# Kernel tuning notes

Hardware: AMD Instinct MI355X
Metric: run time of the kernel (lower is better)

## Reference

```python
import jax, jax.numpy as jnp
import numpy as np

TOPK = 10
HID = 512
RHID = 150
CH = 32


def _gru(x, Wi, Wh, bi, bh):
    """torch nn.GRU (1 layer, batch_first) with gate order r,z,n. x: [B,T,D]."""
    H = Wh.shape[1]
    xi = x @ Wi.T + bi  # [B,T,3H] precompute input projections

    def step(h, xt):
        gh = h @ Wh.T + bh
        r = jax.nn.sigmoid(xt[:, :H] + gh[:, :H])
        z = jax.nn.sigmoid(xt[:, H:2 * H] + gh[:, H:2 * H])
        n = jnp.tanh(xt[:, 2 * H:] + r * gh[:, 2 * H:])
        h_new = (1.0 - z) * n + z * h
        return h_new, h_new

    h0 = jnp.zeros((x.shape[0], H), x.dtype)
    hT, ys = jax.lax.scan(step, h0, jnp.swapaxes(xi, 0, 1))
    return jnp.swapaxes(ys, 0, 1), hT


def reference(window, emb, w_init, w_root, arma_b, Wi1, Wh1, bi1, bh1,
              Wi2, Wh2, bi2, bh2, W_fc, b_fc):
    B, T, N = window.shape
    # --- SingleEmbedding (post-warmup): cosine similarity + per-row top-k ---
    Wn = emb / jnp.clip(jnp.linalg.norm(emb, axis=1, keepdims=True), 1e-8, None)
    A = Wn @ Wn.T
    A = A * (1.0 - jnp.eye(N, dtype=A.dtype))  # fill_diagonal_(0)
    A = jnp.maximum(A, 0.0)                    # clamp(0)
    vals, idx = jax.lax.top_k(A, TOPK)         # [N, TOPK]
    # zero-valued edges kept with weight 0: identical math (zero degree/message contribution)
    src = jnp.repeat(jnp.arange(N), TOPK)      # edge source = row i
    dst = idx.reshape(-1)                      # edge dest = col j
    attr = vals.reshape(-1)
    # --- batch edges over B (offset b*N), then over T (offset t*B*N), as in torch code ---
    boff = jnp.arange(B) * N
    bsrc = (src[None, :] + boff[:, None]).reshape(-1)   # [B*E]
    bdst = (dst[None, :] + boff[:, None]).reshape(-1)
    battr = jnp.tile(attr, B)
    toff = jnp.arange(T) * (B * N)
    fsrc = (bsrc[None, :] + toff[:, None]).reshape(-1)  # [T*B*E]
    fdst = (bdst[None, :] + toff[:, None]).reshape(-1)
    fattr = jnp.tile(battr, T)
    Ntot = B * N * T
    # node layout (b, n, t): flat row = (b*N + n)*T + t  (faithful to torch view order)
    x = jnp.transpose(window, (0, 2, 1)).reshape(Ntot, 1)
    # --- ARMAConv: 1 stack, 1 layer, GELU, gcn_norm without self-loops ---
    deg = jax.ops.segment_sum(fattr, fdst, num_segments=Ntot)
    dinv = jnp.where(deg > 0, jax.lax.rsqrt(jnp.where(deg > 0, deg, 1.0)), 0.0)
    enorm = dinv[fsrc] * fattr * dinv[fdst]
    h = x @ w_init                                            # [Ntot, CH]
    agg = jax.ops.segment_sum(h[fsrc] * enorm[:, None], fdst, num_segments=Ntot)
    out = jax.nn.gelu(agg + x @ w_root + arma_b, approximate=False)
    # --- add node embedding, GRU encode ---
    xt = out.reshape(B, N, T, CH).transpose(0, 2, 1, 3) + emb  # [B,T,N,CH]
    xt = xt.reshape(B, T, N * CH)
    _, h_end = _gru(xt, Wi1, Wh1, bi1, bh1)                   # [B, HID]
    # --- ReconstructionModel: repeat_interleave(T, dim=1).view(B,T,-1) then GRU+fc ---
    hrep = jnp.repeat(h_end, T, axis=1).reshape(B, T, HID)
    dec, _ = _gru(hrep, Wi2, Wh2, bi2, bh2)                   # [B,T,RHID]
    return dec @ W_fc.T + b_fc


def setup_inputs():
    key = jax.random.key(0)
    ks = jax.random.split(key, 10)
    B, T, N = 32, 100, 150
    d_in = N * CH
    return {
        "window": jax.random.normal(ks[0], (B, T, N), jnp.float32),
        "emb": jax.random.normal(ks[1], (N, CH), jnp.float32) * 0.3,
        "w_init": jax.random.normal(ks[2], (1, CH), jnp.float32) * 0.5,
        "w_root": jax.random.normal(ks[3], (1, CH), jnp.float32) * 0.5,
        "arma_b": jnp.zeros((CH,), jnp.float32),
        "Wi1": jax.random.normal(ks[4], (3 * HID, d_in), jnp.float32) * (1.0 / np.sqrt(d_in)),
        "Wh1": jax.random.normal(ks[5], (3 * HID, HID), jnp.float32) * (1.0 / np.sqrt(HID)),
        "bi1": jnp.zeros((3 * HID,), jnp.float32),
        "bh1": jnp.zeros((3 * HID,), jnp.float32),
        "Wi2": jax.random.normal(ks[6], (3 * RHID, HID), jnp.float32) * (1.0 / np.sqrt(HID)),
        "Wh2": jax.random.normal(ks[7], (3 * RHID, RHID), jnp.float32) * (1.0 / np.sqrt(RHID)),
        "bi2": jnp.zeros((3 * RHID,), jnp.float32),
        "bh2": jnp.zeros((3 * RHID,), jnp.float32),
        "W_fc": jax.random.normal(ks[8], (N, RHID), jnp.float32) * (1.0 / np.sqrt(RHID)),
        "b_fc": jnp.zeros((N,), jnp.float32),
    }
```

## Files before the change

kernel.cpp:

```cpp
#include <hip/hip_runtime.h>
#include <hip/hip_fp16.h>
#include <math.h>

typedef _Float16 f16;
typedef _Float16 half8 __attribute__((ext_vector_type(8)));
typedef _Float16 half4 __attribute__((ext_vector_type(4)));
typedef float float4v __attribute__((ext_vector_type(4)));
typedef float float2v __attribute__((ext_vector_type(2)));
typedef unsigned int uint4v __attribute__((ext_vector_type(4)));

#define AS1 __attribute__((address_space(1)))
#define AS3 __attribute__((address_space(3)))

constexpr size_t alup(size_t x){ return (x + 255) & ~(size_t)255; }
constexpr size_t OFF_MT   = 0;
constexpr size_t OFF_DEG  = alup(OFF_MT + 150*150*4);
constexpr size_t OFF_HT0  = alup(OFF_DEG + 150*4);
constexpr size_t OFF_HT1  = alup(OFF_HT0 + (size_t)32*512*4);
constexpr size_t OFF_WI2P = alup(OFF_HT1 + (size_t)32*512*4);
constexpr size_t OFF_WFCP = alup(OFF_WI2P + (size_t)512*512*2);
constexpr size_t OFF_WH2P = alup(OFF_WFCP + (size_t)256*192*2);
constexpr size_t OFF_DECB = alup(OFF_WH2P + (size_t)512*160*2);
constexpr size_t ZONE_END = alup(OFF_DECB + (size_t)3200*192*2);
constexpr size_t OFF_EDST = ZONE_END;
constexpr size_t OFF_EVAL = alup(OFF_EDST + 1500*4);
constexpr size_t OFF_XF   = alup(OFF_EVAL + 1500*4);
constexpr size_t OFF_SS   = alup(OFF_XF + (size_t)480000*4);
constexpr size_t OFF_XT   = alup(OFF_SS + (size_t)480000*4);
constexpr size_t OFF_WI1H = alup(OFF_XT + (size_t)3200*4800*2);
constexpr size_t OFF_XI1  = alup(OFF_WI1H + (size_t)1536*4800*2);
constexpr size_t OFF_U    = alup(OFF_XI1 + (size_t)3200*1536*2);
constexpr size_t OFF_XI2  = alup(OFF_U + (size_t)3200*512*2);

static __device__ __forceinline__ float fsig(float x){ return 1.0f/(1.0f + __expf(-x)); }
static __device__ __forceinline__ float ftanh(float x){
    x = fminf(fmaxf(x, -15.f), 15.f);
    float e = __expf(2.0f*x);
    return (e - 1.0f)/(e + 1.0f);
}

__global__ void k_topk(const float* __restrict__ emb, int* __restrict__ EDST,
                       float* __restrict__ EVAL, float* __restrict__ DEG) {
    __shared__ float WnT[32*152];
    __shared__ float invn[160];
    __shared__ float As[160];
    int tid = threadIdx.x;
    int i = blockIdx.x;
    for (int idx = tid; idx < 4800; idx += 256) {
        int jj = idx >> 5, c = idx & 31;
        WnT[c*152 + jj] = emb[idx];
    }
    __syncthreads();
    if (tid < 150) {
        float s = 0.f;
        #pragma unroll
        for (int c = 0; c < 32; ++c) { float v = WnT[c*152 + tid]; s += v*v; }
        invn[tid] = 1.0f / fmaxf(sqrtf(s), 1e-8f);
    }
    __syncthreads();
    for (int idx = tid; idx < 4800; idx += 256) {
        int jj = idx >> 5, c = idx & 31;
        WnT[c*152 + jj] *= invn[jj];
    }
    __syncthreads();
    int j = tid;
    if (j < 150) {
        float a = 0.f;
        #pragma unroll
        for (int c = 0; c < 32; ++c) a += WnT[c*152 + i] * WnT[c*152 + j];
        a = (j == i) ? 0.f : fmaxf(a, 0.f);
        As[j] = a;
    }
    __syncthreads();
    if (j < 150) {
        float aj = As[j];
        int cnt = 0;
        for (int m = 0; m < 150; ++m) {
            float am = As[m];
            cnt += (am > aj) || (am == aj && m < j);
        }
        if (cnt < 10) {
            EDST[i*10 + cnt] = j;
            EVAL[i*10 + cnt] = aj;
            atomicAdd(&DEG[j], aj);
        }
    }
}

__global__ void k_prep(const int* __restrict__ EDST, const float* __restrict__ EVAL,
                       const float* __restrict__ DEG, float* __restrict__ MT,
                       const float* __restrict__ Wi1, f16* __restrict__ WI1H,
                       const float* __restrict__ Wi2, f16* __restrict__ WI2P,
                       const float* __restrict__ W_fc, f16* __restrict__ WFCP,
                       const float* __restrict__ Wh2, f16* __restrict__ WH2P,
                       const float* __restrict__ window, float* __restrict__ XF) {
    int b = blockIdx.x, tid = threadIdx.x;
    if (b == 0) {
        __shared__ float dinv[160];
        if (tid < 150) {
            float d = DEG[tid];
            dinv[tid] = (d > 0.f) ? rsqrtf(d) : 0.f;
        }
        __syncthreads();
        for (int e = tid; e < 1500; e += 256) {
            int src = e / 10;
            int dst = EDST[e];
            MT[src*150 + dst] = dinv[src] * EVAL[e] * dinv[dst];
        }
    } else if (b < 28801) {
        int idx = (b - 1)*256 + tid;
        WI1H[idx] = (f16)Wi1[idx];
    } else if (b < 29701) {
        int idx = (b - 28801)*256 + tid;
        WI2P[idx] = (f16)Wi2[idx];
    } else if (b < 29789) {
        int idx = (b - 29701)*256 + tid;
        if (idx < 22500) {
            int r = idx / 150, c = idx % 150;
            WFCP[r*192 + c] = (f16)W_fc[idx];
        }
    } else if (b < 30053) {
        int idx = (b - 29789)*256 + tid;
        if (idx < 67500) {
            int r = idx / 150, c = idx % 150;
            WH2P[r*160 + c] = (f16)Wh2[idx];
        }
    } else {
        int idx = (b - 30053)*256 + tid;
        float v = window[idx];
        int bb = idx / 15000;
        int r = idx % 15000;
        int t = r / 150, n = r % 150;
        XF[bb*15000 + n*100 + t] = v;
    }
}

__global__ void k_conv(const float* __restrict__ XF, const float* __restrict__ MT,
                       float* __restrict__ SS) {
    __shared__ float xs[152];
    int tid = threadIdx.x;
    int base = blockIdx.x * 150;
    if (tid < 150) xs[tid] = XF[base + tid];
    __syncthreads();
    if (tid < 150) {
        float s = 0.f;
        for (int m = 0; m < 150; ++m) s += MT[m*150 + tid] * xs[m];
        SS[base + tid] = s;
    }
}

__global__ void k_xt(const float* __restrict__ SS, const float* __restrict__ XF,
                     const float* __restrict__ w_init, const float* __restrict__ w_root,
                     const float* __restrict__ arma_b, const float* __restrict__ emb,
                     f16* __restrict__ xt) {
    __shared__ float ssl[152];
    __shared__ float xfl[152];
    int tid = threadIdx.x;
    int bid = blockIdx.x;
    int b = bid / 100, t = bid % 100;
    if (tid < 150) {
        int f = b*15000 + tid*100 + t;
        ssl[tid] = SS[f];
        xfl[tid] = XF[f];
    }
    __syncthreads();
    for (int e = tid; e < 4800; e += 256) {
        int n = e >> 5, c = e & 31;
        float pre = ssl[n]*w_init[c] + xfl[n]*w_root[c] + arma_b[c];
        float g = 0.5f * pre * (1.0f + erff(pre * 0.70710678118654752f));
        xt[(size_t)bid*4800 + e] = (f16)(g + emb[e]);
    }
}

template <typename TC>
__global__ void k_gemm(const f16* __restrict__ A, const f16* __restrict__ Bm,
                       const float* __restrict__ bias, TC* __restrict__ C,
                       int K, int ldc, int nvalid, int ntm) {
    __shared__ f16 As[128*64];
    __shared__ f16 Bs[128*64];
    int tid = threadIdx.x;
    int lane = tid & 63, wave = tid >> 6;
    int wm = wave >> 1, wn = wave & 1;
    int tm = blockIdx.x % ntm, tn = blockIdx.x / ntm;
    int m0 = tm * 128, n0 = tn * 128;
    int lrow = lane & 15, quad = lane >> 4;

    float4v acc[4][4];
    #pragma unroll
    for (int mi = 0; mi < 4; ++mi)
        #pragma unroll
        for (int ni = 0; ni < 4; ++ni)
            acc[mi][ni] = (float4v){0.f, 0.f, 0.f, 0.f};

    for (int k0 = 0; k0 < K; k0 += 64) {
        #pragma unroll
        for (int i = 0; i < 4; ++i) {
            int cid = i*256 + tid;
            int row = cid >> 3, cq = cid & 7;
            int cbase = cid & ~63;
            const f16* ga = A + (size_t)(m0+row)*K + k0 + cq*8;
            __builtin_amdgcn_global_load_lds((const AS1 void*)ga, (AS3 void*)(As + cbase*8), 16, 0, 0);
            const f16* gb = Bm + (size_t)(n0+row)*K + k0 + cq*8;
            __builtin_amdgcn_global_load_lds((const AS1 void*)gb, (AS3 void*)(Bs + cbase*8), 16, 0, 0);
        }
        __syncthreads();
        #pragma unroll
        for (int kk = 0; kk < 2; ++kk) {
            half8 aF[4], bF[4];
            #pragma unroll
            for (int mi = 0; mi < 4; ++mi)
                aF[mi] = *(const half8*)&As[(wm*64 + mi*16 + lrow)*64 + kk*32 + quad*8];
            #pragma unroll
            for (int ni = 0; ni < 4; ++ni)
                bF[ni] = *(const half8*)&Bs[(wn*64 + ni*16 + lrow)*64 + kk*32 + quad*8];
            #pragma unroll
            for (int mi = 0; mi < 4; ++mi)
                #pragma unroll
                for (int ni = 0; ni < 4; ++ni)
                    acc[mi][ni] = __builtin_amdgcn_mfma_f32_16x16x32_f16(aF[mi], bF[ni], acc[mi][ni], 0, 0, 0);
        }
        __syncthreads();
    }

    #pragma unroll
    for (int ni = 0; ni < 4; ++ni) {
        int gcol = n0 + wn*64 + ni*16 + lrow;
        if (gcol >= nvalid) continue;
        float bv = bias[gcol];
        #pragma unroll
        for (int mi = 0; mi < 4; ++mi) {
            int growb = m0 + wm*64 + mi*16 + quad*4;
            #pragma unroll
            for (int r = 0; r < 4; ++r)
                C[(size_t)(growb + r)*ldc + gcol] = (TC)(acc[mi][ni][r] + bv);
        }
    }
}

__global__ __launch_bounds__(256, 1)
void k_gru1(const f16* __restrict__ xi1, const float* __restrict__ Wh1,
            const float* __restrict__ bh1, unsigned* __restrict__ ht0,
            unsigned* __restrict__ ht1) {
    __shared__ __align__(16) f16 hA[16*640];
    __shared__ float ghs[192];
    int tid = threadIdx.x;
    int g = blockIdx.x & 15;
    int j = blockIdx.x >> 4;
    int b0 = g * 2;
    int lane = tid & 63, wave = tid >> 6;
    int lrow = lane & 15, quad = lane >> 4;

    half8 Bf0[16], Bf1[16];
    if (wave < 3) {
        #pragma unroll
        for (int tile = 0; tile < 2; ++tile) {
            int rr = (wave*2 + tile)*16 + lrow;
            int grow = (rr >> 5)*512 + (j << 5) + (rr & 31);
            const float* wp = Wh1 + (size_t)grow*512 + quad*8;
            #pragma unroll
            for (int k0 = 0; k0 < 16; ++k0) {
                float4v w0 = *(const float4v*)(wp + k0*32);
                float4v w1 = *(const float4v*)(wp + k0*32 + 4);
                half8 hb;
                hb[0]=(f16)w0[0]; hb[1]=(f16)w0[1]; hb[2]=(f16)w0[2]; hb[3]=(f16)w0[3];
                hb[4]=(f16)w1[0]; hb[5]=(f16)w1[1]; hb[6]=(f16)w1[2]; hb[7]=(f16)w1[3];
                if (tile == 0) Bf0[k0] = hb; else Bf1[k0] = hb;
            }
        }
    }

    float hold = 0.f, bhr = 0.f, bhz = 0.f, bhn = 0.f;
    f16 xir = (f16)0.f, xiz = (f16)0.f, xin = (f16)0.f;
    size_t xb = 0;
    if (tid < 64) {
        int bl = tid >> 5, i = tid & 31;
        int col = (j << 5) + i;
        bhr = bh1[col]; bhz = bh1[512 + col]; bhn = bh1[1024 + col];
        xb = (size_t)((b0 + bl)*100)*1536 + col;
        xir = xi1[xb]; xiz = xi1[xb + 512]; xin = xi1[xb + 1024];
    }
    int sbl = tid >> 7;
    int kb  = (tid & 127) << 2;

    for (int t = 0; t < 100; ++t) {
        const unsigned* cur = (t & 1) ? ht1 : ht0;
        unsigned* nxt = (t & 1) ? ht0 : ht1;
        {
            const unsigned* p = cur + (size_t)(b0 + sbl)*512 + kb;
            uint4v A4;
            unsigned tagw = (unsigned)t << 16;
            for (;;) {
                asm volatile("global_load_dwordx4 %0, %1, off sc0 sc1\n\ts_waitcnt vmcnt(0)"
                             : "=v"(A4) : "v"(p) : "memory");
                if ((A4[0] & 0xffff0000u) == tagw && (A4[1] & 0xffff0000u) == tagw &&
                    (A4[2] & 0xffff0000u) == tagw && (A4[3] & 0xffff0000u) == tagw) break;
                __builtin_amdgcn_s_sleep(1);
            }
            union { unsigned short s[4]; half4 h; } cv;
            cv.s[0] = (unsigned short)A4[0]; cv.s[1] = (unsigned short)A4[1];
            cv.s[2] = (unsigned short)A4[2]; cv.s[3] = (unsigned short)A4[3];
            *(half4*)&hA[(kb >> 5)*640 + sbl*40 + (kb & 31)] = cv.h;
        }
        __syncthreads();

        if (wave < 3) {
            float4v a0a = (float4v){0.f,0.f,0.f,0.f}, a0b = a0a, a1a = a0a, a1b = a0a;
            const f16* aB = &hA[lrow*40 + quad*8];
            #pragma unroll
            for (int k0 = 0; k0 < 16; k0 += 2) {
                half8 a0 = *(const half8*)(aB + k0*640);
                half8 a1 = *(const half8*)(aB + (k0+1)*640);
                a0a = __builtin_amdgcn_mfma_f32_16x16x32_f16(a0, Bf0[k0], a0a, 0, 0, 0);
                a1a = __builtin_amdgcn_mfma_f32_16x16x32_f16(a0, Bf1[k0], a1a, 0, 0, 0);
                a0b = __builtin_amdgcn_mfma_f32_16x16x32_f16(a1, Bf0[k0+1], a0b, 0, 0, 0);
                a1b = __builtin_amdgcn_mfma_f32_16x16x32_f16(a1, Bf1[k0+1], a1b, 0, 0, 0);
            }
            if (lane < 16) {
                int n0 = wave*2, n1 = n0 + 1;
                ghs[n0*16 + lane]      = a0a[0] + a0b[0];
                ghs[96 + n0*16 + lane] = a0a[1] + a0b[1];
                ghs[n1*16 + lane]      = a1a[0] + a1b[0];
                ghs[96 + n1*16 + lane] = a1a[1] + a1b[1];
            }
        }
        __syncthreads();

        if (tid < 64) {
            int bl = tid >> 5, i = tid & 31;
            float xr_ = (float)xir, xz_ = (float)xiz, xn_ = (float)xin;
            int tn = (t < 99) ? t + 1 : 99;
            size_t xo = xb + (size_t)tn*1536;
            xir = xi1[xo]; xiz = xi1[xo + 512]; xin = xi1[xo + 1024];
            float gr = ghs[bl*96 + i]      + bhr;
            float gz = ghs[bl*96 + 32 + i] + bhz;
            float gn = ghs[bl*96 + 64 + i] + bhn;
            float r = fsig(xr_ + gr);
            float z = fsig(xz_ + gz);
            float n = ftanh(xn_ + r*gn);
            float hnew = (1.f - z)*n + z*hold;
            hold = hnew;
            union { f16 h; unsigned short s; } hb; hb.h = (f16)hnew;
            unsigned pk = ((unsigned)(t + 1) << 16) | (unsigned)hb.s;
            __hip_atomic_store(nxt + (size_t)(b0 + bl)*512 + (j << 5) + i, pk,
                               __ATOMIC_RELAXED, __HIP_MEMORY_SCOPE_AGENT);
        }
    }
}

__global__ void k_build_u(const unsigned* __restrict__ ht0, f16* __restrict__ u) {
    int idx = blockIdx.x * blockDim.x + threadIdx.x;
    if (idx >= 32*100*512) return;
    int b = idx / 51200;
    int r = idx % 51200;
    int t = r >> 9, k = r & 511;
    union { unsigned short s; f16 h; } cv;
    cv.s = (unsigned short)ht0[(b << 9) + ((t*512 + k) / 100)];
    u[idx] = cv.h;
}

__global__ __launch_bounds__(256, 1)
void k_gru2(const f16* __restrict__ xi2, const f16* __restrict__ wh2p,
            const float* __restrict__ bh2, f16* __restrict__ decb) {
    __shared__ __align__(16) f16 hA[5*640];
    __shared__ float ghs[512];
    int tid = threadIdx.x;
    int b = blockIdx.x;
    int lane = tid & 63, wave = tid >> 6;
    int lrow = lane & 15, quad = lane >> 4;

    for (int i = tid; i < 5*640; i += 256) hA[i] = (f16)0.f;

    half8 Bf[8][5];
    #pragma unroll
    for (int tt = 0; tt < 8; ++tt) {
        int rn = (wave*8 + tt)*16 + lrow;
        const f16* wp = wh2p + (size_t)rn*160 + quad*8;
        #pragma unroll
        for (int k0 = 0; k0 < 5; ++k0)
            Bf[tt][k0] = *(const half8*)(wp + k0*32);
    }

    float hold = 0.f, bhr = 0.f, bhz = 0.f, bhn = 0.f;
    f16 xr = (f16)0.f, xz = (f16)0.f, xn = (f16)0.f;
    size_t xbase = (size_t)b * 100 * 512;
    if (tid < 150) {
        bhr = bh2[tid]; bhz = bh2[150 + tid]; bhn = bh2[300 + tid];
        xr = xi2[xbase + tid]; xz = xi2[xbase + 150 + tid]; xn = xi2[xbase + 300 + tid];
    }
    __syncthreads();

    for (int t = 0; t < 100; ++t) {
        float4v acc[8];
        #pragma unroll
        for (int tt = 0; tt < 8; ++tt) acc[tt] = (float4v){0.f,0.f,0.f,0.f};
        #pragma unroll
        for (int k0 = 0; k0 < 5; ++k0) {
            half8 a = *(const half8*)&hA[k0*640 + lrow*40 + quad*8];
            #pragma unroll
            for (int tt = 0; tt < 8; ++tt)
                acc[tt] = __builtin_amdgcn_mfma_f32_16x16x32_f16(a, Bf[tt][k0], acc[tt], 0, 0, 0);
        }
        if (lane < 16) {
            #pragma unroll
            for (int tt = 0; tt < 8; ++tt)
                ghs[(wave*8 + tt)*16 + lane] = acc[tt][0];
        }
        __syncthreads();

        if (tid < 150) {
            float r = fsig((float)xr + ghs[tid] + bhr);
            float z = fsig((float)xz + ghs[150 + tid] + bhz);
            float n = ftanh((float)xn + r*(ghs[300 + tid] + bhn));
            float hnew = (1.f - z)*n + z*hold;
            hold = hnew;
            f16 hh = (f16)hnew;
            hA[(tid >> 5)*640 + (tid & 31)] = hh;
            decb[((size_t)b*100 + t)*192 + tid] = hh;
            int tn = (t < 99) ? t + 1 : 99;
            size_t xo = xbase + (size_t)tn*512;
            xr = xi2[xo + tid]; xz = xi2[xo + 150 + tid]; xn = xi2[xo + 300 + tid];
        }
        __syncthreads();
    }
}

extern "C" void kernel_launch(void* const* d_in, const int* in_sizes, int n_in,
                              void* d_out, int out_size, void* d_ws, size_t ws_size,
                              hipStream_t stream) {
    const float* window = (const float*)d_in[0];
    const float* emb    = (const float*)d_in[1];
    const float* w_init = (const float*)d_in[2];
    const float* w_root = (const float*)d_in[3];
    const float* arma_b = (const float*)d_in[4];
    const float* Wi1    = (const float*)d_in[5];
    const float* Wh1    = (const float*)d_in[6];
    const float* bi1    = (const float*)d_in[7];
    const float* bh1    = (const float*)d_in[8];
    const float* Wi2    = (const float*)d_in[9];
    const float* Wh2    = (const float*)d_in[10];
    const float* bi2    = (const float*)d_in[11];
    const float* bh2    = (const float*)d_in[12];
    const float* W_fc   = (const float*)d_in[13];
    const float* b_fc   = (const float*)d_in[14];
    float* out = (float*)d_out;

    char* ws = (char*)d_ws;
    float*    MT   = (float*)(ws + OFF_MT);
    float*    DEG  = (float*)(ws + OFF_DEG);
    unsigned* HT0  = (unsigned*)(ws + OFF_HT0);
    unsigned* HT1  = (unsigned*)(ws + OFF_HT1);
    f16*      WI2P = (f16*)  (ws + OFF_WI2P);
    f16*      WFCP = (f16*)  (ws + OFF_WFCP);
    f16*      WH2P = (f16*)  (ws + OFF_WH2P);
    f16*      DECB = (f16*)  (ws + OFF_DECB);
    int*      EDST = (int*)  (ws + OFF_EDST);
    float*    EVAL = (float*)(ws + OFF_EVAL);
    float*    XF   = (float*)(ws + OFF_XF);
    float*    SS   = (float*)(ws + OFF_SS);
    f16*      XT   = (f16*)  (ws + OFF_XT);
    f16*      WI1H = (f16*)  (ws + OFF_WI1H);
    f16*      XI1H = (f16*)  (ws + OFF_XI1);
    f16*      UB   = (f16*)  (ws + OFF_U);
    f16*      XI2H = (f16*)  (ws + OFF_XI2);

    hipMemsetAsync(d_ws, 0, ZONE_END, stream);

    k_topk<<<150, 256, 0, stream>>>(emb, EDST, EVAL, DEG);

    k_prep<<<31928, 256, 0, stream>>>(EDST, EVAL, DEG, MT,
                                      Wi1, WI1H, Wi2, WI2P, W_fc, WFCP,
                                      Wh2, WH2P, window, XF);

    k_conv<<<3200, 256, 0, stream>>>(XF, MT, SS);
    k_xt<<<3200, 256, 0, stream>>>(SS, XF, w_init, w_root, arma_b, emb, XT);

    k_gemm<f16><<<25*12, 256, 0, stream>>>(XT, WI1H, bi1, XI1H, 4800, 1536, 1536, 25);

    k_gru1<<<256, 256, 0, stream>>>(XI1H, Wh1, bh1, HT0, HT1);

    k_build_u<<<(32*100*512 + 255)/256, 256, 0, stream>>>(HT0, UB);

    k_gemm<f16><<<25*4, 256, 0, stream>>>(UB, WI2P, bi2, XI2H, 512, 512, 450, 25);

    k_gru2<<<32, 256, 0, stream>>>(XI2H, WH2P, bh2, DECB);

    k_gemm<float><<<25*2, 256, 0, stream>>>(DECB, WFCP, b_fc, out, 192, 150, 150, 25);

    (void)in_sizes; (void)n_in; (void)out_size; (void)ws_size;
}
```

Before: 544.1 us.

## Replace GRU2 input GEMM with prefix-sum segment formulation; shrink GEMM M-tile

The second GRU's input is built from a repeated hidden state: each length-512 row of U is piecewise constant, taking only about 6-7 distinct values. The change precomputes prefix sums of Wi2 along K, then computes each xi2 entry as a few segment differences times h values. This removes the build_u kernel and the 512x512 GEMM. Separately, the generic GEMM M-tile drops from 128 to 64 rows, doubling block count for more parallelism on the large Wi1 GEMM. Risks are fp32 prefix-sum cancellation error and a serial 512-step prefix loop run on only 2 blocks in prep.

```diff
diff --git a/kernel.cpp b/kernel.cpp
--- a/kernel.cpp
+++ b/kernel.cpp
@@ -17,20 +17,19 @@
 constexpr size_t OFF_DEG  = alup(OFF_MT + 150*150*4);
 constexpr size_t OFF_HT0  = alup(OFF_DEG + 150*4);
 constexpr size_t OFF_HT1  = alup(OFF_HT0 + (size_t)32*512*4);
-constexpr size_t OFF_WI2P = alup(OFF_HT1 + (size_t)32*512*4);
-constexpr size_t OFF_WFCP = alup(OFF_WI2P + (size_t)512*512*2);
+constexpr size_t OFF_WFCP = alup(OFF_HT1 + (size_t)32*512*4);
 constexpr size_t OFF_WH2P = alup(OFF_WFCP + (size_t)256*192*2);
 constexpr size_t OFF_DECB = alup(OFF_WH2P + (size_t)512*160*2);
 constexpr size_t ZONE_END = alup(OFF_DECB + (size_t)3200*192*2);
 constexpr size_t OFF_EDST = ZONE_END;
 constexpr size_t OFF_EVAL = alup(OFF_EDST + 1500*4);
-constexpr size_t OFF_XF   = alup(OFF_EVAL + 1500*4);
+constexpr size_t OFF_PT   = alup(OFF_EVAL + 1500*4);
+constexpr size_t OFF_XF   = alup(OFF_PT + (size_t)513*452*4);
 constexpr size_t OFF_SS   = alup(OFF_XF + (size_t)480000*4);
 constexpr size_t OFF_XT   = alup(OFF_SS + (size_t)480000*4);
 constexpr size_t OFF_WI1H = alup(OFF_XT + (size_t)3200*4800*2);
 constexpr size_t OFF_XI1  = alup(OFF_WI1H + (size_t)1536*4800*2);
-constexpr size_t OFF_U    = alup(OFF_XI1 + (size_t)3200*1536*2);
-constexpr size_t OFF_XI2  = alup(OFF_U + (size_t)3200*512*2);
+constexpr size_t OFF_XI2  = alup(OFF_XI1 + (size_t)3200*1536*2);
 
 static __device__ __forceinline__ float fsig(float x){ return 1.0f/(1.0f + __expf(-x)); }
 static __device__ __forceinline__ float ftanh(float x){
@@ -90,10 +89,10 @@
 __global__ void k_prep(const int* __restrict__ EDST, const float* __restrict__ EVAL,
                        const float* __restrict__ DEG, float* __restrict__ MT,
                        const float* __restrict__ Wi1, f16* __restrict__ WI1H,
-                       const float* __restrict__ Wi2, f16* __restrict__ WI2P,
                        const float* __restrict__ W_fc, f16* __restrict__ WFCP,
                        const float* __restrict__ Wh2, f16* __restrict__ WH2P,
-                       const float* __restrict__ window, float* __restrict__ XF) {
+                       const float* __restrict__ window, float* __restrict__ XF,
+                       const float* __restrict__ Wi2, float* __restrict__ PT) {
     int b = blockIdx.x, tid = threadIdx.x;
     if (b == 0) {
         __shared__ float dinv[160];
@@ -110,28 +109,35 @@
     } else if (b < 28801) {
         int idx = (b - 1)*256 + tid;
         WI1H[idx] = (f16)Wi1[idx];
-    } else if (b < 29701) {
+    } else if (b < 28889) {
         int idx = (b - 28801)*256 + tid;
-        WI2P[idx] = (f16)Wi2[idx];
-    } else if (b < 29789) {
-        int idx = (b - 29701)*256 + tid;
         if (idx < 22500) {
             int r = idx / 150, c = idx % 150;
             WFCP[r*192 + c] = (f16)W_fc[idx];
         }
-    } else if (b < 30053) {
-        int idx = (b - 29789)*256 + tid;
+    } else if (b < 29153) {
+        int idx = (b - 28889)*256 + tid;
         if (idx < 67500) {
             int r = idx / 150, c = idx % 150;
             WH2P[r*160 + c] = (f16)Wh2[idx];
         }
-    } else {
-        int idx = (b - 30053)*256 + tid;
+    } else if (b < 31028) {
+        int idx = (b - 29153)*256 + tid;
         float v = window[idx];
         int bb = idx / 15000;
         int r = idx % 15000;
         int t = r / 150, n = r % 150;
         XF[bb*15000 + n*100 + t] = v;
+    } else {
+        int o = (b - 31028)*256 + tid;
+        if (o < 450) {
+            float run = 0.f;
+            PT[o] = 0.f;
+            for (int k = 0; k < 512; ++k) {
+                run += Wi2[o*512 + k];
+                PT[(size_t)(k+1)*452 + o] = run;
+            }
+        }
     }
 }
 
@@ -176,45 +182,51 @@
 __global__ void k_gemm(const f16* __restrict__ A, const f16* __restrict__ Bm,
                        const float* __restrict__ bias, TC* __restrict__ C,
                        int K, int ldc, int nvalid, int ntm) {
-    __shared__ f16 As[128*64];
+    __shared__ f16 As[64*64];
     __shared__ f16 Bs[128*64];
     int tid = threadIdx.x;
     int lane = tid & 63, wave = tid >> 6;
     int wm = wave >> 1, wn = wave & 1;
     int tm = blockIdx.x % ntm, tn = blockIdx.x / ntm;
-    int m0 = tm * 128, n0 = tn * 128;
+    int m0 = tm * 64, n0 = tn * 128;
     int lrow = lane & 15, quad = lane >> 4;
 
-    float4v acc[4][4];
+    float4v acc[2][4];
     #pragma unroll
-    for (int mi = 0; mi < 4; ++mi)
+    for (int mi = 0; mi < 2; ++mi)
         #pragma unroll
         for (int ni = 0; ni < 4; ++ni)
             acc[mi][ni] = (float4v){0.f, 0.f, 0.f, 0.f};
 
     for (int k0 = 0; k0 < K; k0 += 64) {
         #pragma unroll
-        for (int i = 0; i < 4; ++i) {
+        for (int i = 0; i < 2; ++i) {
             int cid = i*256 + tid;
             int row = cid >> 3, cq = cid & 7;
             int cbase = cid & ~63;
             const f16* ga = A + (size_t)(m0+row)*K + k0 + cq*8;
             __builtin_amdgcn_global_load_lds((const AS1 void*)ga, (AS3 void*)(As + cbase*8), 16, 0, 0);
+        }
+        #pragma unroll
+        for (int i = 0; i < 4; ++i) {
+            int cid = i*256 + tid;
+            int row = cid >> 3, cq = cid & 7;
+            int cbase = cid & ~63;
             const f16* gb = Bm + (size_t)(n0+row)*K + k0 + cq*8;
             __builtin_amdgcn_global_load_lds((const AS1 void*)gb, (AS3 void*)(Bs + cbase*8), 16, 0, 0);
         }
         __syncthreads();
         #pragma unroll
         for (int kk = 0; kk < 2; ++kk) {
-            half8 aF[4], bF[4];
-            #pragma unroll
-            for (int mi = 0; mi < 4; ++mi)
-                aF[mi] = *(const half8*)&As[(wm*64 + mi*16 + lrow)*64 + kk*32 + quad*8];
+            half8 aF[2], bF[4];
+            #pragma unroll
+            for (int mi = 0; mi < 2; ++mi)
+                aF[mi] = *(const half8*)&As[(wm*32 + mi*16 + lrow)*64 + kk*32 + quad*8];
             #pragma unroll
             for (int ni = 0; ni < 4; ++ni)
                 bF[ni] = *(const half8*)&Bs[(wn*64 + ni*16 + lrow)*64 + kk*32 + quad*8];
             #pragma unroll
-            for (int mi = 0; mi < 4; ++mi)
+            for (int mi = 0; mi < 2; ++mi)
                 #pragma unroll
                 for (int ni = 0; ni < 4; ++ni)
                     acc[mi][ni] = __builtin_amdgcn_mfma_f32_16x16x32_f16(aF[mi], bF[ni], acc[mi][ni], 0, 0, 0);
@@ -228,8 +240,8 @@
         if (gcol >= nvalid) continue;
         float bv = bias[gcol];
         #pragma unroll
-        for (int mi = 0; mi < 4; ++mi) {
-            int growb = m0 + wm*64 + mi*16 + quad*4;
+        for (int mi = 0; mi < 2; ++mi) {
+            int growb = m0 + wm*32 + mi*16 + quad*4;
             #pragma unroll
             for (int r = 0; r < 4; ++r)
                 C[(size_t)(growb + r)*ldc + gcol] = (TC)(acc[mi][ni][r] + bv);
@@ -347,15 +359,39 @@
     }
 }
 
-__global__ void k_build_u(const unsigned* __restrict__ ht0, f16* __restrict__ u) {
-    int idx = blockIdx.x * blockDim.x + threadIdx.x;
-    if (idx >= 32*100*512) return;
-    int b = idx / 51200;
-    int r = idx % 51200;
-    int t = r >> 9, k = r & 511;
-    union { unsigned short s; f16 h; } cv;
-    cv.s = (unsigned short)ht0[(b << 9) + ((t*512 + k) / 100)];
-    u[idx] = cv.h;
+__global__ void k_xi2(const unsigned* __restrict__ ht0, const float* __restrict__ PT,
+                      const float* __restrict__ bi2, f16* __restrict__ xi2) {
+    __shared__ float hs[512];
+    int tid = threadIdx.x;
+    int bid = blockIdx.x;
+    int b = bid / 100, t = bid % 100;
+    {
+        union { unsigned short s; f16 h; } c1, c2;
+        c1.s = (unsigned short)ht0[(b << 9) + tid];
+        c2.s = (unsigned short)ht0[(b << 9) + tid + 256];
+        hs[tid] = (float)c1.h;
+        hs[tid + 256] = (float)c2.h;
+    }
+    __syncthreads();
+    int base = t * 512;
+    int m0 = base / 100;
+    #pragma unroll
+    for (int q = 0; q < 2; ++q) {
+        int o = tid + q*256;
+        if (o < 450) {
+            float acc = bi2[o];
+            #pragma unroll
+            for (int s = 0; s < 7; ++s) {
+                int klo = (m0 + s)*100 - base;     klo = klo < 0 ? 0 : klo;
+                int khi = (m0 + s + 1)*100 - base; khi = khi > 512 ? 512 : khi;
+                if (klo < khi) {
+                    float seg = PT[(size_t)khi*452 + o] - PT[(size_t)klo*452 + o];
+                    acc += hs[m0 + s] * seg;
+                }
+            }
+            xi2[(size_t)bid*512 + o] = (f16)acc;
+        }
+    }
 }
 
 __global__ __launch_bounds__(256, 1)
@@ -449,42 +485,39 @@
     float*    DEG  = (float*)(ws + OFF_DEG);
     unsigned* HT0  = (unsigned*)(ws + OFF_HT0);
     unsigned* HT1  = (unsigned*)(ws + OFF_HT1);
-    f16*      WI2P = (f16*)  (ws + OFF_WI2P);
     f16*      WFCP = (f16*)  (ws + OFF_WFCP);
     f16*      WH2P = (f16*)  (ws + OFF_WH2P);
     f16*      DECB = (f16*)  (ws + OFF_DECB);
     int*      EDST = (int*)  (ws + OFF_EDST);
     float*    EVAL = (float*)(ws + OFF_EVAL);
+    float*    PT   = (float*)(ws + OFF_PT);
     float*    XF   = (float*)(ws + OFF_XF);
     float*    SS   = (float*)(ws + OFF_SS);
     f16*      XT   = (f16*)  (ws + OFF_XT);
     f16*      WI1H = (f16*)  (ws + OFF_WI1H);
     f16*      XI1H = (f16*)  (ws + OFF_XI1);
-    f16*      UB   = (f16*)  (ws + OFF_U);
     f16*      XI2H = (f16*)  (ws + OFF_XI2);
 
     hipMemsetAsync(d_ws, 0, ZONE_END, stream);
 
     k_topk<<<150, 256, 0, stream>>>(emb, EDST, EVAL, DEG);
 
-    k_prep<<<31928, 256, 0, stream>>>(EDST, EVAL, DEG, MT,
-                                      Wi1, WI1H, Wi2, WI2P, W_fc, WFCP,
-                                      Wh2, WH2P, window, XF);
+    k_prep<<<31030, 256, 0, stream>>>(EDST, EVAL, DEG, MT,
+                                      Wi1, WI1H, W_fc, WFCP, Wh2, WH2P,
+                                      window, XF, Wi2, PT);
 
     k_conv<<<3200, 256, 0, stream>>>(XF, MT, SS);
     k_xt<<<3200, 256, 0, stream>>>(SS, XF, w_init, w_root, arma_b, emb, XT);
 
-    k_gemm<f16><<<25*12, 256, 0, stream>>>(XT, WI1H, bi1, XI1H, 4800, 1536, 1536, 25);
+    k_gemm<f16><<<50*12, 256, 0, stream>>>(XT, WI1H, bi1, XI1H, 4800, 1536, 1536, 50);
 
     k_gru1<<<256, 256, 0, stream>>>(XI1H, Wh1, bh1, HT0, HT1);
 
-    k_build_u<<<(32*100*512 + 255)/256, 256, 0, stream>>>(HT0, UB);
-
-    k_gemm<f16><<<25*4, 256, 0, stream>>>(UB, WI2P, bi2, XI2H, 512, 512, 450, 25);
+    k_xi2<<<3200, 256, 0, stream>>>(HT0, PT, bi2, XI2H);
 
     k_gru2<<<32, 256, 0, stream>>>(XI2H, WH2P, bh2, DECB);
 
-    k_gemm<float><<<25*2, 256, 0, stream>>>(DECB, WFCP, b_fc, out, 192, 150, 150, 25);
+    k_gemm<float><<<50*2, 256, 0, stream>>>(DECB, WFCP, b_fc, out, 192, 150, 150, 50);
 
     (void)in_sizes; (void)n_in; (void)out_size; (void)ws_size;
 }
```

Measured after the change: 541.0 us. About the same (-0.6%).
